# Kernel optimization log

Hardware: AMD Instinct MI355X
Metric: run time of the kernel (lower is better)

## Reference

```python
import jax, jax.numpy as jnp
import numpy as np


def setup_inputs() -> dict:
    key = jax.random.key(0)
    k1, k2 = jax.random.split(key)
    B, C, H, W = 8, 64, 32, 32
    K = 8192
    x = jax.random.normal(k1, (B, C, H, W), dtype=jnp.float32)
    codebook = jax.random.normal(k2, (K, C), dtype=jnp.float32)
    return {"x": x, "codebook": codebook}


def reference(x, codebook):
    """Faithful JAX version of VQVAE.quantize().

    x:        [B, C, H, W] latent (output of pre_quant_conv)
    codebook: [K, C] embedding weight
    Returns (quant_out [B,C,H,W], commitment_loss, codebook_loss, indices [B,H,W]).
    """
    B, C, H, W = x.shape
    # [B, H, W, C] -> [B, N, C]
    xf = jnp.transpose(x, (0, 2, 3, 1)).reshape(B, H * W, C)

    # Squared pairwise distances (argmin of cdist == argmin of squared dist).
    x2 = jnp.sum(xf * xf, axis=-1, keepdims=True)            # [B, N, 1]
    e2 = jnp.sum(codebook * codebook, axis=-1)               # [K]
    xe = jnp.einsum('bnc,kc->bnk', xf, codebook)             # [B, N, K]
    d2 = x2 + e2[None, None, :] - 2.0 * xe                   # [B, N, K]
    idx = jnp.argmin(d2, axis=-1)                            # [B, N]

    quant = codebook[idx.reshape(-1)]                        # [B*N, C]
    xflat = xf.reshape(-1, C)                                # [B*N, C]

    commitment_loss = jnp.mean((jax.lax.stop_gradient(quant) - xflat) ** 2)
    codebook_loss = jnp.mean((quant - jax.lax.stop_gradient(xflat)) ** 2)

    # Straight-through estimator.
    quant_st = xflat + jax.lax.stop_gradient(quant - xflat)
    quant_out = jnp.transpose(quant_st.reshape(B, H, W, C), (0, 3, 1, 2))
    indices = idx.reshape(B, H, W)
    return quant_out, commitment_loss, codebook_loss, indices
```

## Files before the change

### kernel.cpp

```cpp
#include <hip/hip_runtime.h>


#define N_PTS   8192
#define K_CODES 8192
#define C_DIM   64
#define HWSZ    1024
#define QOUT_N  524288
#define SPLITS  32

#define WS_XS    0
#define WS_CBS   3145728
#define WS_E2H   6291456
#define WS_PACK  6324224
#define WS_PART  8421376

typedef __attribute__((ext_vector_type(8))) short short8;
typedef __attribute__((ext_vector_type(4))) float floatx4;

__device__ __forceinline__ unsigned short bf16_rne(float f) {
    unsigned u = __float_as_uint(f);
    return (unsigned short)((u + 0x7FFFu + ((u >> 16) & 1u)) >> 16);
}
__device__ __forceinline__ float bf16_val(unsigned short h) {
    return __uint_as_float(((unsigned)h) << 16);
}
__device__ __forceinline__ void split3(float v, unsigned short& h,
                                       unsigned short& m, unsigned short& l) {
    h = bf16_rne(v);
    float r1 = v - bf16_val(h);
    m = bf16_rne(r1);
    float r2 = r1 - bf16_val(m);
    l = bf16_rne(r2);
}

__global__ __launch_bounds__(256)
void vq_prep_kernel(const float* __restrict__ x,
                    const float* __restrict__ cb,
                    unsigned short* __restrict__ xS,
                    unsigned short* __restrict__ cbS,
                    float* __restrict__ e2h)
{
    const int bx  = blockIdx.x;
    const int tid = threadIdx.x;

    if (bx < 32) {
        const int k = bx * 256 + tid;
        const float* row = cb + k * C_DIM;
        float s = 0.0f;
        #pragma unroll
        for (int g = 0; g < 8; ++g) {
            float4 a = *(const float4*)(row + g * 8);
            float4 b = *(const float4*)(row + g * 8 + 4);
            float vv[8] = {a.x, a.y, a.z, a.w, b.x, b.y, b.z, b.w};
            unsigned short h8[8], m8[8], l8[8];
            #pragma unroll
            for (int j = 0; j < 8; ++j) {
                s = fmaf(vv[j], vv[j], s);
                split3(vv[j], h8[j], m8[j], l8[j]);
            }
            *(uint4*)(cbS + ((size_t)(0 * 8 + g) * 8192 + k) * 8) = *(const uint4*)h8;
            *(uint4*)(cbS + ((size_t)(1 * 8 + g) * 8192 + k) * 8) = *(const uint4*)m8;
            *(uint4*)(cbS + ((size_t)(2 * 8 + g) * 8192 + k) * 8) = *(const uint4*)l8;
        }
        e2h[k] = 0.5f * s;
    } else {
        const int u = bx - 32;
        const int b = u >> 3, g = u & 7;
        const float* xb = x + (size_t)(b * C_DIM + g * 8) * HWSZ;
        float v[4][8];
        #pragma unroll
        for (int cq = 0; cq < 8; ++cq) {
            float4 t4 = *(const float4*)(xb + cq * HWSZ + tid * 4);
            v[0][cq] = t4.x; v[1][cq] = t4.y; v[2][cq] = t4.z; v[3][cq] = t4.w;
        }
        #pragma unroll
        for (int j = 0; j < 4; ++j) {
            unsigned short h8[8], m8[8], l8[8];
            #pragma unroll
            for (int cq = 0; cq < 8; ++cq)
                split3(v[j][cq], h8[cq], m8[cq], l8[cq]);
            const size_t n = (size_t)b * 1024 + tid * 4 + j;
            *(uint4*)(xS + ((size_t)(0 * 8 + g) * 8192 + n) * 8) = *(const uint4*)h8;
            *(uint4*)(xS + ((size_t)(1 * 8 + g) * 8192 + n) * 8) = *(const uint4*)m8;
            *(uint4*)(xS + ((size_t)(2 * 8 + g) * 8192 + n) * 8) = *(const uint4*)l8;
        }
    }
}

__device__ __forceinline__ void loadB(const unsigned short* __restrict__ cbS,
                                      const float* __restrict__ e2h,
                                      int code, int quad,
                                      short8 bf[3][2], float& me2)
{
    #pragma unroll
    for (int p = 0; p < 3; ++p)
        #pragma unroll
        for (int s = 0; s < 2; ++s) {
            int g = s * 4 + quad;
            bf[p][s] = *(const short8*)(cbS + ((size_t)(p * 8 + g) * 8192 + code) * 8);
        }
    me2 = -e2h[code];
}

__device__ __forceinline__ void computeTile(const short8 af[4][3][2],
                                            const short8 bf[3][2],
                                            float me2, int code,
                                            float bestv[4][4], int besti[4][4])
{
    floatx4 acc[4];
    #pragma unroll
    for (int t = 0; t < 4; ++t) acc[t] = (floatx4){me2, me2, me2, me2};

    #pragma unroll
    for (int s = 0; s < 2; ++s) {
        #pragma unroll
        for (int t = 0; t < 4; ++t)
            acc[t] = __builtin_amdgcn_mfma_f32_16x16x32_bf16(af[t][0][s], bf[0][s], acc[t], 0, 0, 0);
        #pragma unroll
        for (int t = 0; t < 4; ++t)
            acc[t] = __builtin_amdgcn_mfma_f32_16x16x32_bf16(af[t][0][s], bf[1][s], acc[t], 0, 0, 0);
        #pragma unroll
        for (int t = 0; t < 4; ++t)
            acc[t] = __builtin_amdgcn_mfma_f32_16x16x32_bf16(af[t][1][s], bf[0][s], acc[t], 0, 0, 0);
        #pragma unroll
        for (int t = 0; t < 4; ++t)
            acc[t] = __builtin_amdgcn_mfma_f32_16x16x32_bf16(af[t][0][s], bf[2][s], acc[t], 0, 0, 0);
        #pragma unroll
        for (int t = 0; t < 4; ++t)
            acc[t] = __builtin_amdgcn_mfma_f32_16x16x32_bf16(af[t][2][s], bf[0][s], acc[t], 0, 0, 0);
        #pragma unroll
        for (int t = 0; t < 4; ++t)
            acc[t] = __builtin_amdgcn_mfma_f32_16x16x32_bf16(af[t][1][s], bf[1][s], acc[t], 0, 0, 0);
    }

    #pragma unroll
    for (int t = 0; t < 4; ++t)
        #pragma unroll
        for (int r = 0; r < 4; ++r) {
            float sc = acc[t][r];
            bool gt = sc > bestv[t][r];
            bestv[t][r] = gt ? sc   : bestv[t][r];
            besti[t][r] = gt ? code : besti[t][r];
        }
}

__global__ __launch_bounds__(256, 2)
void vq_argmin_kernel(const unsigned short* __restrict__ xS,
                      const unsigned short* __restrict__ cbS,
                      const float* __restrict__ e2h,
                      unsigned long long* __restrict__ packedS)
{
    __shared__ unsigned long long red[256][17];
    const int tid   = threadIdx.x;
    const int lane  = tid & 63;
    const int w     = tid >> 6;
    const int col   = lane & 15;
    const int quad  = lane >> 4;
    const int mb    = blockIdx.x;
    const int split = blockIdx.y;
    const int m0    = mb * 256 + w * 64;
    const int nb0   = split * 256;

    short8 af[4][3][2];
    #pragma unroll
    for (int t = 0; t < 4; ++t) {
        int pt = m0 + t * 16 + col;
        #pragma unroll
        for (int p = 0; p < 3; ++p)
            #pragma unroll
            for (int s = 0; s < 2; ++s) {
                int g = s * 4 + quad;
                af[t][p][s] = *(const short8*)(xS + ((size_t)(p * 8 + g) * 8192 + pt) * 8);
            }
    }

    float bestv[4][4];
    int   besti[4][4];
    #pragma unroll
    for (int t = 0; t < 4; ++t)
        #pragma unroll
        for (int r = 0; r < 4; ++r) {
            bestv[t][r] = __uint_as_float(0xFF800000u);
            besti[t][r] = 0;
        }

    short8 b0[3][2], b1[3][2];
    float  e0, e1;
    loadB(cbS, e2h, nb0 + col, quad, b0, e0);

    for (int nt = 0; nt < 16; nt += 2) {
        loadB(cbS, e2h, nb0 + (nt + 1) * 16 + col, quad, b1, e1);
        computeTile(af, b0, e0, nb0 + nt * 16 + col, bestv, besti);
        if (nt + 2 < 16)
            loadB(cbS, e2h, nb0 + (nt + 2) * 16 + col, quad, b0, e0);
        computeTile(af, b1, e1, nb0 + (nt + 1) * 16 + col, bestv, besti);
    }

    #pragma unroll
    for (int t = 0; t < 4; ++t)
        #pragma unroll
        for (int r = 0; r < 4; ++r) {
            unsigned u = __float_as_uint(-bestv[t][r]);
            u = ((int)u < 0) ? ~u : (u | 0x80000000u);
            unsigned long long p = ((unsigned long long)u << 32) | (unsigned)besti[t][r];
            red[w * 64 + t * 16 + quad * 4 + r][col] = p;
        }
    __syncthreads();
    unsigned long long v = red[tid][0];
    #pragma unroll
    for (int c = 1; c < 16; ++c) {
        unsigned long long q = red[tid][c];
        v = (q < v) ? q : v;
    }
    packedS[(size_t)split * N_PTS + mb * 256 + tid] = v;
}

__global__ __launch_bounds__(256)
void vq_gather_kernel(const float* __restrict__ x,
                      const float* __restrict__ cb,
                      const unsigned long long* __restrict__ packedS,
                      float* __restrict__ out,
                      float* __restrict__ part)
{
    __shared__ int sidx[64];
    const int tid  = threadIdx.x;
    const int lane = tid & 63;
    const int qd   = tid >> 6;
    const int n0   = blockIdx.x * 64;
    const int n    = n0 + lane;

    if (qd == 0) {
        unsigned long long v = packedS[n];
        #pragma unroll
        for (int s = 1; s < SPLITS; ++s) {
            unsigned long long q = packedS[(size_t)s * N_PTS + n];
            v = (q < v) ? q : v;
        }
        int idx = (int)(v & 0xFFFFFFFFull);
        sidx[lane] = idx;
        out[QOUT_N + 2 + n] = (float)idx;
    }
    __syncthreads();

    const int idx = sidx[lane];
    const int c0  = qd * 16;
    const int b   = n >> 10;
    const int hw  = n & 1023;
    const float* xb = x   + (size_t)b * (C_DIM * HWSZ) + hw;
    float*       ob = out + (size_t)b * (C_DIM * HWSZ) + hw;

    float s = 0.0f;
    #pragma unroll
    for (int c4 = 0; c4 < 4; ++c4) {
        float4 q = *(const float4*)(cb + (size_t)idx * C_DIM + c0 + c4 * 4);
        float qa[4] = {q.x, q.y, q.z, q.w};
        #pragma unroll
        for (int j = 0; j < 4; ++j) {
            int c = c0 + c4 * 4 + j;
            float xv = xb[c * HWSZ];
            float d  = qa[j] - xv;
            s = fmaf(d, d, s);
            ob[c * HWSZ] = xv + d;
        }
    }

    #pragma unroll
    for (int off = 32; off > 0; off >>= 1) s += __shfl_down(s, off, 64);
    if (lane == 0) part[blockIdx.x * 4 + qd] = s;
}

__global__ __launch_bounds__(256)
void vq_final_kernel(const float* __restrict__ part, float* __restrict__ out)
{
    __shared__ float w[4];
    float s = part[threadIdx.x] + part[threadIdx.x + 256];
    #pragma unroll
    for (int off = 32; off > 0; off >>= 1) s += __shfl_down(s, off, 64);
    if ((threadIdx.x & 63) == 0) w[threadIdx.x >> 6] = s;
    __syncthreads();
    if (threadIdx.x == 0) {
        float m = (w[0] + w[1] + w[2] + w[3]) * (1.0f / (float)QOUT_N);
        out[QOUT_N]     = m;
        out[QOUT_N + 1] = m;
    }
}

extern "C" void kernel_launch(void* const* d_in, const int* in_sizes, int n_in,
                              void* d_out, int out_size, void* d_ws, size_t ws_size,
                              hipStream_t stream)
{
    const float* x  = (const float*)d_in[0];
    const float* cb = (const float*)d_in[1];
    float* out = (float*)d_out;
    char*  ws  = (char*)d_ws;
    (void)ws_size;

    unsigned short* xS  = (unsigned short*)(ws + WS_XS);
    unsigned short* cbS = (unsigned short*)(ws + WS_CBS);
    float* e2h = (float*)(ws + WS_E2H);
    unsigned long long* packedS = (unsigned long long*)(ws + WS_PACK);
    float* part = (float*)(ws + WS_PART);

    vq_prep_kernel<<<96, 256, 0, stream>>>(x, cb, xS, cbS, e2h);
    vq_argmin_kernel<<<dim3(N_PTS / 256, SPLITS), 256, 0, stream>>>(xS, cbS, e2h, packedS);
    vq_gather_kernel<<<128, 256, 0, stream>>>(x, cb, packedS, out, part);
    vq_final_kernel<<<1, 256, 0, stream>>>(part, out);
}
```

Measured before the change: 107.7 us.

## Stage codebook tiles in LDS with double-buffered global_load_lds shared across waves

The argmin kernel no longer has each wave load its own copy of the bf16-split codebook fragments and e2 terms from global memory. It now copies 64-code chunks into a double-buffered LDS area with direct global-to-LDS loads, and all four waves read from that area. This removes the 4x redundant global/L2 traffic for the B operand. In exchange it adds block-wide barriers per chunk and LDS read traffic. The reduction scratch now reuses the same LDS buffer.

```diff
diff --git a/kernel.cpp b/kernel.cpp
--- a/kernel.cpp
+++ b/kernel.cpp
@@ -31,6 +31,16 @@
     m = bf16_rne(r1);
     float r2 = r1 - bf16_val(m);
     l = bf16_rne(r2);
+}
+__device__ __forceinline__ void cp16(const void* g, void* l) {
+    __builtin_amdgcn_global_load_lds(
+        (const __attribute__((address_space(1))) void*)g,
+        (__attribute__((address_space(3))) void*)l, 16, 0, 0);
+}
+__device__ __forceinline__ void cp4(const void* g, void* l) {
+    __builtin_amdgcn_global_load_lds(
+        (const __attribute__((address_space(1))) void*)g,
+        (__attribute__((address_space(3))) void*)l, 4, 0, 0);
 }
 
 __global__ __launch_bounds__(256)
@@ -87,26 +97,24 @@
     }
 }
 
-__device__ __forceinline__ void loadB(const unsigned short* __restrict__ cbS,
-                                      const float* __restrict__ e2h,
-                                      int code, int quad,
-                                      short8 bf[3][2], float& me2)
-{
+#define SEG_SHORTS 512
+#define BUF_SHORTS 12416
+
+__device__ __forceinline__ void computeTileLDS(const short8 af[4][3][2],
+                                               const unsigned short* __restrict__ bsrc,
+                                               int tl, int quad, int col, int code,
+                                               float bestv[4][4], int besti[4][4])
+{
+    short8 bf[3][2];
     #pragma unroll
     for (int p = 0; p < 3; ++p)
         #pragma unroll
         for (int s = 0; s < 2; ++s) {
-            int g = s * 4 + quad;
-            bf[p][s] = *(const short8*)(cbS + ((size_t)(p * 8 + g) * 8192 + code) * 8);
-        }
-    me2 = -e2h[code];
-}
-
-__device__ __forceinline__ void computeTile(const short8 af[4][3][2],
-                                            const short8 bf[3][2],
-                                            float me2, int code,
-                                            float bestv[4][4], int besti[4][4])
-{
+            int seg = p * 8 + s * 4 + quad;
+            bf[p][s] = *(const short8*)(bsrc + seg * SEG_SHORTS + (tl * 16 + col) * 8);
+        }
+    float me2 = -((const float*)(bsrc + 24 * SEG_SHORTS))[tl * 16 + col];
+
     floatx4 acc[4];
     #pragma unroll
     for (int t = 0; t < 4; ++t) acc[t] = (floatx4){me2, me2, me2, me2};
@@ -150,7 +158,8 @@
                       const float* __restrict__ e2h,
                       unsigned long long* __restrict__ packedS)
 {
-    __shared__ unsigned long long red[256][17];
+    __shared__ __align__(16) unsigned short sBuf[2][BUF_SHORTS];
+
     const int tid   = threadIdx.x;
     const int lane  = tid & 63;
     const int w     = tid >> 6;
@@ -184,18 +193,34 @@
             besti[t][r] = 0;
         }
 
-    short8 b0[3][2], b1[3][2];
-    float  e0, e1;
-    loadB(cbS, e2h, nb0 + col, quad, b0, e0);
-
-    for (int nt = 0; nt < 16; nt += 2) {
-        loadB(cbS, e2h, nb0 + (nt + 1) * 16 + col, quad, b1, e1);
-        computeTile(af, b0, e0, nb0 + nt * 16 + col, bestv, besti);
-        if (nt + 2 < 16)
-            loadB(cbS, e2h, nb0 + (nt + 2) * 16 + col, quad, b0, e0);
-        computeTile(af, b1, e1, nb0 + (nt + 1) * 16 + col, bestv, besti);
-    }
-
+    auto stage = [&](int k0, int buf) {
+        unsigned short* dst = &sBuf[buf][0];
+        #pragma unroll
+        for (int i = 0; i < 6; ++i) {
+            int f   = tid + i * 256;
+            int seg = f >> 6;
+            int l   = f & 63;
+            cp16(cbS + ((size_t)seg * 8192 + k0 + l) * 8,
+                 dst + seg * SEG_SHORTS + l * 8);
+        }
+        if (tid < 64)
+            cp4(e2h + k0 + tid, (float*)(dst + 24 * SEG_SHORTS) + tid);
+    };
+
+    stage(nb0, 0);
+    __syncthreads();
+
+    for (int ch = 0; ch < 4; ++ch) {
+        if (ch + 1 < 4) stage(nb0 + (ch + 1) * 64, (ch + 1) & 1);
+        const unsigned short* bsrc = &sBuf[ch & 1][0];
+        #pragma unroll
+        for (int tl = 0; tl < 4; ++tl)
+            computeTileLDS(af, bsrc, tl, quad, col,
+                           nb0 + ch * 64 + tl * 16 + col, bestv, besti);
+        __syncthreads();
+    }
+
+    unsigned long long* red = (unsigned long long*)&sBuf[0][0];
     #pragma unroll
     for (int t = 0; t < 4; ++t)
         #pragma unroll
@@ -203,13 +228,13 @@
             unsigned u = __float_as_uint(-bestv[t][r]);
             u = ((int)u < 0) ? ~u : (u | 0x80000000u);
             unsigned long long p = ((unsigned long long)u << 32) | (unsigned)besti[t][r];
-            red[w * 64 + t * 16 + quad * 4 + r][col] = p;
+            red[(w * 64 + t * 16 + quad * 4 + r) * 17 + col] = p;
         }
     __syncthreads();
-    unsigned long long v = red[tid][0];
+    unsigned long long v = red[tid * 17];
     #pragma unroll
     for (int c = 1; c < 16; ++c) {
-        unsigned long long q = red[tid][c];
+        unsigned long long q = red[tid * 17 + c];
         v = (q < v) ? q : v;
     }
     packedS[(size_t)split * N_PTS + mb * 256 + tid] = v;
```

Result: faster. 103.8 us (-3.6%).
